# Kernel tuning notes

Hardware: AMD Instinct MI355X
Metric: run time of the kernel (lower is better)

## Reference

```python
import jax, jax.numpy as jnp
import numpy as np

F, HE, HD, A = 128, 512, 512, 256
B, T = 32, 512

def _uniform(key, shape, k):
    return jax.random.uniform(key, shape, jnp.float32, -k, k)

def setup_inputs() -> dict:
    key = jax.random.key(0)
    ks = jax.random.split(key, 20)
    ke = 1.0 / np.sqrt(HE)
    kd = 1.0 / np.sqrt(HD)
    ka = 1.0 / np.sqrt(A)
    kf = 1.0 / np.sqrt(F)
    return {
        "x": jax.random.normal(ks[0], (B, T, F), jnp.float32),
        # encoder LSTM (torch gate order i,f,g,o)
        "enc_Wih": _uniform(ks[1], (4 * HE, F), ke),
        "enc_Whh": _uniform(ks[2], (4 * HE, HE), ke),
        "enc_bih": _uniform(ks[3], (4 * HE,), ke),
        "enc_bhh": _uniform(ks[4], (4 * HE,), ke),
        # attention
        "Wenc_w": _uniform(ks[5], (A, HE), 1.0 / np.sqrt(HE)),
        "Wenc_b": _uniform(ks[6], (A,), 1.0 / np.sqrt(HE)),
        "Wdec_w": _uniform(ks[7], (A, HD), kd),
        "Wdec_b": _uniform(ks[8], (A,), kd),
        "V_w": _uniform(ks[9], (1, A), ka),
        "V_b": _uniform(ks[10], (1,), ka),
        "attn_bias": _uniform(ks[11], (A,), kd),
        # decoder LSTMCell: input size HD+HE
        "dec_Wih": _uniform(ks[12], (4 * HD, HD + HE), kd),
        "dec_Whh": _uniform(ks[13], (4 * HD, HD), kd),
        "dec_bih": _uniform(ks[14], (4 * HD,), kd),
        "dec_bhh": _uniform(ks[15], (4 * HD,), kd),
    }

def _lstm_step(xw, h, c, Whh, bias, H):
    # xw = x @ Wih.T precomputed; bias = bih + bhh
    z = xw + h @ Whh.T + bias
    i, f, g, o = jnp.split(z, 4, axis=-1)
    i, f, o = jax.nn.sigmoid(i), jax.nn.sigmoid(f), jax.nn.sigmoid(o)
    g = jnp.tanh(g)
    c_new = f * c + i * g
    h_new = o * jnp.tanh(c_new)
    return h_new, c_new

def reference(x, enc_Wih, enc_Whh, enc_bih, enc_bhh,
              Wenc_w, Wenc_b, Wdec_w, Wdec_b, V_w, V_b, attn_bias,
              dec_Wih, dec_Whh, dec_bih, dec_bhh):
    nb, nt, _ = x.shape
    # ---- encoder LSTM ----
    xw = jnp.einsum('btf,gf->btg', x, enc_Wih)  # [B,T,4HE]
    enc_bias = enc_bih + enc_bhh
    def enc_step(carry, xw_t):
        h, c = carry
        h, c = _lstm_step(xw_t, h, c, enc_Whh, enc_bias, HE)
        return (h, c), h
    h0 = jnp.zeros((nb, HE), x.dtype)
    c0 = jnp.zeros((nb, HE), x.dtype)
    _, enc_states = jax.lax.scan(enc_step, (h0, c0), jnp.swapaxes(xw, 0, 1))
    enc_states = jnp.swapaxes(enc_states, 0, 1)  # [B,T,HE]

    # ---- initial decoder step: zero input, zero state ----
    dec_bias = dec_bih + dec_bhh
    z0 = jnp.broadcast_to(dec_bias, (nb, 4 * HD))
    i, f, g, o = jnp.split(z0, 4, axis=-1)
    cdec = jax.nn.sigmoid(i) * jnp.tanh(g)
    hdec = jax.nn.sigmoid(o) * jnp.tanh(cdec)

    # precompute encoder projection for attention (math identical to per-step)
    enc_proj = jnp.einsum('bte,ae->bta', enc_states, Wenc_w) + Wenc_b  # [B,T,A]

    def dec_step(carry, _):
        h, c = carry
        dscore = h @ Wdec_w.T + Wdec_b  # [B,A]
        align = jnp.tanh(enc_proj + dscore[:, None, :] + attn_bias)  # [B,T,A]
        logits = jnp.einsum('bta,a->bt', align, V_w[0]) + V_b[0]
        w = jax.nn.softmax(logits, axis=-1)  # [B,T]
        ctx = jnp.einsum('bt,bte->be', w, enc_states)  # [B,HE]
        dec_in = jnp.concatenate([ctx, h], axis=-1)
        h, c = _lstm_step(dec_in @ dec_Wih.T, h, c, dec_Whh, dec_bias, HD)
        return (h, c), h
    _, outs = jax.lax.scan(dec_step, (hdec, cdec), None, length=nt)
    return jnp.swapaxes(outs, 0, 1)  # [B,T,HD]
```

## Files before the change

### kernel.cpp

```cpp
#include <hip/hip_runtime.h>
#include <stdint.h>

#define DEV __device__ __forceinline__

namespace {

constexpr int kT = 512, kB = 32, kF = 128, kHE = 512, kHD = 512, kA = 256;

typedef _Float16 f16;
typedef _Float16 h4 __attribute__((ext_vector_type(4)));
typedef unsigned long long u64;

constexpr size_t oWdecC  = 0;
constexpr size_t oWdWH   = oWdecC + 1048576;
constexpr size_t oEncSt  = oWdWH + 65536;
constexpr size_t oEncPr  = oEncSt + (size_t)kB*kT*kHE;
constexpr size_t oHdec   = oEncPr + (size_t)kB*kT*kA;
constexpr size_t oCtx    = oHdec + 3ull*kB*kHD;
constexpr size_t oDen    = oCtx + 3ull*kB*kHE;
constexpr size_t oScp    = oDen + 96;
constexpr size_t oEbias  = oScp + (size_t)kB*16*kA;
constexpr size_t oDbias  = oEbias + 2048;
constexpr size_t oAb2    = oDbias + 2048;
constexpr size_t oCtr    = oAb2 + 256;
constexpr size_t oHenc   = oCtr + 2048;
constexpr size_t oCtxP   = oEncSt;
constexpr size_t oDenP   = oEncSt + 3ull*32*16*512;

constexpr float kScale = 1.0f/64.0f;

DEV float frcp(float x){ return __builtin_amdgcn_rcpf(x); }
DEV float fsig(float x){ return frcp(1.f + __expf(-x)); }
DEV float ftanh(float x){ return 1.f - 2.f*frcp(__expf(2.f*x) + 1.f); }

DEV float ld_na(const float* p){ return __hip_atomic_load((float*)p, __ATOMIC_RELAXED, __HIP_MEMORY_SCOPE_AGENT); }
DEV void  st_na(float* p, float v){ __hip_atomic_store(p, v, __ATOMIC_RELAXED, __HIP_MEMORY_SCOPE_AGENT); }
DEV int   ld_ni(const int* p){ return __hip_atomic_load((int*)p, __ATOMIC_RELAXED, __HIP_MEMORY_SCOPE_AGENT); }
DEV void  st_ni(int* p, int v){ __hip_atomic_store(p, v, __ATOMIC_RELAXED, __HIP_MEMORY_SCOPE_AGENT); }
DEV float2 ld_na2(const float* p){
  u64 v = __hip_atomic_load((const u64*)p, __ATOMIC_RELAXED, __HIP_MEMORY_SCOPE_AGENT);
  union { u64 u; float2 f; } cv; cv.u = v; return cv.f;
}
DEV void st_na2(float* p, float2 v){
  union { float2 f; u64 u; } cv; cv.f = v;
  __hip_atomic_store((u64*)p, cv.u, __ATOMIC_RELAXED, __HIP_MEMORY_SCOPE_AGENT);
}

DEV void wait_slots(const int* base, int cnt, int tgt, int* abortf){
  if (threadIdx.x < 64){
    int lane = threadIdx.x;
    int guard = 0;
    for (;;){
      int ok = 1;
      for (int i = lane; i < cnt; i += 64) ok &= (ld_ni(base + i) >= tgt);
      if (__all(ok)) break;
      if (ld_ni(abortf) != 0) break;
      if (++guard > (1<<21)){ st_ni(abortf, 1); break; }
      __builtin_amdgcn_s_sleep(1);
    }
  }
  __syncthreads();
}
DEV void wait_count(const int* p, int tgt, int* abortf){
  if (threadIdx.x < 64){
    int guard = 0;
    for (;;){
      if (ld_ni(p) >= tgt) break;
      if (ld_ni(abortf) != 0) break;
      if (++guard > (1<<21)){ st_ni(abortf, 1); break; }
      __builtin_amdgcn_s_sleep(2);
    }
  }
  __syncthreads();
}
DEV void stamp_slot(int* slot, int v){
  __syncthreads();
  if (threadIdx.x == 0) st_ni(slot, v);
}

}

__global__ __launch_bounds__(256) void init_kernel(
    const float* __restrict__ eBih, const float* __restrict__ eBhh,
    const float* __restrict__ WdecW, const float* __restrict__ WdecB, const float* __restrict__ attnB,
    const float* __restrict__ dWih, const float* __restrict__ dWhh,
    const float* __restrict__ dBih, const float* __restrict__ dBhh,
    float* __restrict__ ws)
{
  float* whc = ws + oWdecC;
  f16* wdwh  = (f16*)(ws + oWdWH);
  float* hdec  = ws + oHdec;
  float* ebias = ws + oEbias;
  float* dbias = ws + oDbias;
  float* ab2w  = ws + oAb2;
  float* henc  = ws + oHenc;
  const int gid = blockIdx.x*256 + threadIdx.x;
  const int stride = gridDim.x*256;
  for (int i=gid; i<2048*512; i+=stride){
    int col = i>>9, k = i&511;
    whc[i] = dWih[((size_t)col<<10) + 512 + k] + dWhh[((size_t)col<<9) + k];
  }
  for (int i=gid; i<256*512; i+=stride)  wdwh[i] = (f16)WdecW[i];
  for (int i=gid; i<2048; i+=stride){ ebias[i] = eBih[i]+eBhh[i]; dbias[i] = dBih[i]+dBhh[i]; }
  for (int i=gid; i<256; i+=stride)  ab2w[i] = WdecB[i]+attnB[i];
  for (int i=gid; i<2*kB*kHE; i+=stride) henc[i] = 0.f;
  for (int i=gid; i<kB*kHD; i+=stride){
    int e = i & 511;
    float zi = dBih[e]+dBhh[e];
    float zg = dBih[1024+e]+dBhh[1024+e];
    float zo = dBih[1536+e]+dBhh[1536+e];
    float c0 = fsig(zi)*ftanh(zg);
    hdec[i] = fsig(zo)*ftanh(c0);
  }
}

__global__ __launch_bounds__(256, 1) void enc_kernel(
    const float* __restrict__ x, const float* __restrict__ eWih,
    const float* __restrict__ eWhh, float* __restrict__ ws)
{
  constexpr int WP = 644;
  constexpr int XP = 648;
  __shared__ float wsm[32*WP];
  __shared__ float xh[8*XP];
  __shared__ float zs[8][32];
  const float* ebias = ws + oEbias;
  float* encst = ws + oEncSt;
  float* henc  = ws + oHenc;
  int* ctr = (int*)(ws + oCtr);
  int* abortf = ctr;
  int* slotE = ctr + 1600;

  const int tid = threadIdx.x, bid = blockIdx.x;
  const int q = bid >> 6, j = bid & 63;
  const int b0 = q*8, e0 = j*8;

  for (int i = tid; i < 32*640; i += 256){
    int r = i / 640, k = i - r*640;
    int gate = r >> 3, el = r & 7;
    int grow = gate*kHE + e0 + el;
    float v = (k < kF) ? eWih[(size_t)grow*kF + k] : eWhh[(size_t)grow*kHE + (k - kF)];
    wsm[r*WP + k] = v;
  }
  const int b_l = tid >> 5, row = tid & 31;
  const float biasr = ebias[(row>>3)*kHE + e0 + (row&7)];
  const int b_p = tid >> 3, e_p = tid & 7;
  float creg = 0.f;
  __syncthreads();

  int p = 0;
  for (int t = 0; t < kT; ++t){
    {
      int bl2 = tid >> 5, q4 = tid & 31;
      *(float4*)(&xh[bl2*XP + 4*q4]) = ((const float4*)(x + ((size_t)(b0+bl2)*kT + t)*kF))[q4];
    }
    float a0=0.f, a1=0.f, a2=0.f, a3=0.f;
    {
      const float4* wr = (const float4*)(&wsm[row*WP]);
      const float4* xr = (const float4*)(&xh[b_l*XP]);
      #pragma unroll 8
      for (int kq = 0; kq < 32; ++kq){
        float4 w = wr[kq], v = xr[kq];
        a0 += w.x*v.x; a1 += w.y*v.y; a2 += w.z*v.z; a3 += w.w*v.w;
      }
    }
    wait_slots(slotE + q*64, 64, t, abortf);
    #pragma unroll
    for (int i = 0; i < 4; ++i){
      int idx = tid + 256*i;
      int bl2 = idx >> 7, q4 = idx & 127;
      const float* hsrc = henc + (size_t)p*kB*kHE + (size_t)(b0+bl2)*kHE + 4*q4;
      float2 h01 = ld_na2(hsrc), h23 = ld_na2(hsrc + 2);
      *(float4*)(&xh[bl2*XP + kF + 4*q4]) = make_float4(h01.x, h01.y, h23.x, h23.y);
    }
    __syncthreads();
    {
      const float4* wr = (const float4*)(&wsm[row*WP]);
      const float4* xr = (const float4*)(&xh[b_l*XP]);
      #pragma unroll 8
      for (int kq = 32; kq < 160; ++kq){
        float4 w = wr[kq], v = xr[kq];
        a0 += w.x*v.x; a1 += w.y*v.y; a2 += w.z*v.z; a3 += w.w*v.w;
      }
      zs[b_l][row] = (a0+a1)+(a2+a3) + biasr;
    }
    __syncthreads();
    if (tid < 64){
      float zi = zs[b_p][0*8 + e_p];
      float zf = zs[b_p][1*8 + e_p];
      float zg = zs[b_p][2*8 + e_p];
      float zo = zs[b_p][3*8 + e_p];
      float c2 = fsig(zf)*creg + fsig(zi)*ftanh(zg);
      creg = c2;
      float h = fsig(zo)*ftanh(c2);
      int b = b0 + b_p, e = e0 + e_p;
      st_na(&henc[(size_t)(p^1)*kB*kHE + (size_t)b*kHE + e], h);
      encst[((size_t)b*kT + t)*kHE + e] = h;
    }
    stamp_slot(&slotE[q*64 + j], t+1);
    p ^= 1;
  }
}

__global__ __launch_bounds__(256) void encproj_kernel(
    const float* __restrict__ WencW, const float* __restrict__ WencB,
    float* __restrict__ ws)
{
  const float* encst = ws + oEncSt;
  float* encpr = ws + oEncPr;
  __shared__ float4 et[32][32];
  const int tid = threadIdx.x, bid = blockIdx.x;
  const int r0 = bid*32;
  float acc[32];
  #pragma unroll
  for (int i=0;i<32;++i) acc[i]=0.f;
  for (int kt=0; kt<4; ++kt){
    #pragma unroll
    for (int i2=0;i2<4;++i2){
      int q = tid + i2*256;
      int row = q>>5, qi = q&31;
      et[row][qi] = ((const float4*)(encst + ((size_t)(r0+row))*kHE + kt*128))[qi];
    }
    __syncthreads();
    const float4* wv = (const float4*)(WencW + (size_t)tid*kHE + kt*128);
    #pragma unroll 1
    for (int q=0;q<32;++q){
      float4 w = wv[q];
      #pragma unroll
      for (int i=0;i<32;++i){
        float4 e4 = et[i][q];
        acc[i] += e4.x*w.x + e4.y*w.y + e4.z*w.z + e4.w*w.w;
      }
    }
    __syncthreads();
  }
  float bb = WencB[tid];
  #pragma unroll
  for (int i=0;i<32;++i) encpr[((size_t)(r0+i))*kA + tid] = acc[i] + bb;
}

namespace {
struct SA  { float h[32]; float sc[256]; float lw[32]; };
struct SC  { float xt[16][520]; float zb[128][2]; };
struct __align__(16) SmemDec {
  float wsl[8][1028];
  float v[256];
  SA a;
  SC c;
};
}

__global__ __launch_bounds__(256, 2) void dec_kernel(
    const float* __restrict__ Vw, const float* __restrict__ dWih,
    float* __restrict__ out, float* __restrict__ ws)
{
  __shared__ SmemDec sm;
  const int tid = threadIdx.x, bid = blockIdx.x;
  const float* whc = ws + oWdecC;
  const f16* wdwh  = (const f16*)(ws + oWdWH);
  const float* encst = ws + oEncSt;
  const float* encpr = ws + oEncPr;
  float* hdec = ws + oHdec;
  float* ctxb = ws + oCtx;
  float* den  = ws + oDen;
  float* scp  = ws + oScp;
  float* ctxp = ws + oCtxP;
  float* denp = ws + oDenP;
  const float* dbias = ws + oDbias;
  const float* ab2w  = ws + oAb2;
  int* ctr   = (int*)(ws + oCtr);
  int* abortf = ctr;
  int* startc = ctr + 16;
  int* slotC = ctr + 64;
  int* slotA = ctr + 576;
  int* slotB = ctr + 1088;
  int* slotR = ctr + 1856;

  const int bA = bid >> 4, tc = bid & 15, t0a = tc*32;
  const int half = bid >> 8, ecp = bid & 255, e0c = ecp*2;
  const bool isR = (tc == 0);
  const int col_l = tid & 127, ksC = tid >> 7;
  const int e_lC = col_l & 1, gateC = (col_l>>1)&3, b_lC = col_l>>3;
  const int wrow = gateC*2 + e_lC;

  for (int i = tid; i < 8*1024; i += 256){
    int rr = i >> 10, k = i & 1023;
    int col = (rr>>1)*kHD + e0c + (rr&1);
    float v = (k < 512) ? dWih[(size_t)col*1024 + k] : whc[(size_t)col*512 + (k-512)];
    sm.wsl[rr][k] = v;
  }
  sm.v[tid] = Vw[tid];

  h4 wA[8];
  { const h4* wv0 = (const h4*)(wdwh + (size_t)tid*kHD + t0a);
    #pragma unroll
    for (int q=0;q<8;++q) wA[q] = wv0[q]; }
  const int tl = tid>>3, as = tid&7;
  float4 eprR[8];
  { const float* eb2 = encpr + ((size_t)bA*kT + t0a + tl)*kA + as*4;
    #pragma unroll
    for (int q=0;q<8;++q) eprR[q] = *(const float4*)(eb2 + q*32); }
  float2 ev[32];
  { const float* eb = encst + ((size_t)bA*kT + t0a)*kHE + 2*tid;
    #pragma unroll
    for (int j=0;j<32;++j) ev[j] = *(const float2*)(eb + (size_t)j*kHE); }

  const float ab2r = ab2w[tid];
  float cregD=0, dbi=0, dbf=0, dbg=0, dbo=0;
  if (tid < 32){
    int e = e0c + (tid&1);
    dbi = dbias[e]; dbf = dbias[512+e]; dbg = dbias[1024+e]; dbo = dbias[1536+e];
    cregD = fsig(dbi)*ftanh(dbg);
  }
  __syncthreads();
  if (tid == 0) atomicAdd(startc, 1);
  wait_count(startc, 512, abortf);

  int r = 0;
  for (int t=0; t<kT; ++t){
    const int rn = (r==2) ? 0 : r+1;
    wait_slots(slotC + (bA>>4)*256 + tc*16, 16, t, abortf);
    if (tid < 32) sm.a.h[tid] = ld_na(hdec + (size_t)r*kB*kHD + (size_t)bA*kHD + t0a + tid);
    __syncthreads();
    {
      float sp = 0.f;
      #pragma unroll
      for (int q=0;q<8;++q){
        h4 w = wA[q];
        sp += (float)w.x*sm.a.h[q*4+0] + (float)w.y*sm.a.h[q*4+1]
            + (float)w.z*sm.a.h[q*4+2] + (float)w.w*sm.a.h[q*4+3];
      }
      st_na(&scp[((size_t)bA*16 + tc)*kA + tid], sp);
    }
    stamp_slot(&slotA[bA*16 + tc], t+1);
    wait_slots(slotA + bA*16, 16, t+1, abortf);
    {
      float sc = ab2r;
      #pragma unroll
      for (int j=0;j<16;++j) sc += ld_na(&scp[((size_t)bA*16 + j)*kA + tid]);
      sm.a.sc[tid] = sc;
    }
    __syncthreads();
    {
      float acc = 0.f;
      #pragma unroll
      for (int q=0;q<8;++q){
        int a0 = q*32 + as*4;
        float4 e4 = eprR[q];
        acc += sm.v[a0+0]*ftanh(e4.x + sm.a.sc[a0+0]);
        acc += sm.v[a0+1]*ftanh(e4.y + sm.a.sc[a0+1]);
        acc += sm.v[a0+2]*ftanh(e4.z + sm.a.sc[a0+2]);
        acc += sm.v[a0+3]*ftanh(e4.w + sm.a.sc[a0+3]);
      }
      acc += __shfl_down(acc, 4, 8);
      acc += __shfl_down(acc, 2, 8);
      acc += __shfl_down(acc, 1, 8);
      if (as == 0) sm.a.lw[tl] = __expf(acc) * kScale;
    }
    __syncthreads();
    {
      float c0=0.f, c1=0.f;
      #pragma unroll
      for (int j=0;j<32;++j){
        float w = sm.a.lw[j];
        c0 += w*ev[j].x; c1 += w*ev[j].y;
      }
      st_na2(&ctxp[(((size_t)r*kB + bA)*16 + tc)*kHE + 2*tid], make_float2(c0, c1));
      if (tid == 0){
        float ds = 0.f;
        #pragma unroll
        for (int j=0;j<32;++j) ds += sm.a.lw[j];
        st_na(&denp[((size_t)r*kB + bA)*16 + tc], ds);
      }
    }
    stamp_slot(&slotB[bA*16 + tc], t+1);
    if (isR){
      wait_slots(slotB + bA*16, 16, t+1, abortf);
      {
        const float* pb = ctxp + ((size_t)r*kB + bA)*16*kHE + 2*tid;
        float s0=0.f, s1=0.f;
        #pragma unroll
        for (int j=0;j<16;++j){
          float2 p = ld_na2(pb + (size_t)j*kHE);
          s0 += p.x; s1 += p.y;
        }
        st_na2(&ctxb[((size_t)r*kB + bA)*kHE + 2*tid], make_float2(s0, s1));
        float d = (tid < 16) ? ld_na(&denp[((size_t)r*kB + bA)*16 + tid]) : 0.f;
        d += __shfl_down(d, 8, 16);
        d += __shfl_down(d, 4, 16);
        d += __shfl_down(d, 2, 16);
        d += __shfl_down(d, 1, 16);
        if (tid == 0) st_na(&den[r*kB + bA], d);
      }
      stamp_slot(&slotR[bA], t+1);
    }
    wait_slots(slotC + half*256, 256, t, abortf);
    float acch = 0.f;
    {
      const float* hbase = hdec + (size_t)r*kB*kHD + (size_t)(half*16)*kHD + 2*tid;
      float2 hu[16];
      #pragma unroll
      for (int b=0;b<16;++b) hu[b] = ld_na2(hbase + (size_t)b*kHD);
      #pragma unroll
      for (int b=0;b<16;++b) *(float2*)(&sm.c.xt[b][2*tid]) = hu[b];
      __syncthreads();
      #pragma unroll
      for (int kc=2; kc<4; ++kc){
        const float4* wc4 = (const float4*)(&sm.wsl[wrow][kc*256 + ksC*128]);
        const float4* xv  = (const float4*)(&sm.c.xt[b_lC][(kc-2)*256 + ksC*128]);
        float a0=0.f, a1=0.f, a2=0.f, a3=0.f;
        #pragma unroll 8
        for (int q=0;q<32;++q){
          float4 w = wc4[q], v = xv[q];
          a0 += w.x*v.x; a1 += w.y*v.y; a2 += w.z*v.z; a3 += w.w*v.w;
        }
        acch += (a0+a1)+(a2+a3);
      }
      __syncthreads();
    }
    wait_slots(slotR + half*16, 16, t+1, abortf);
    {
      const float rv = frcp(ld_na(&den[r*kB + half*16 + b_lC]));
      const float* cbase = ctxb + (size_t)r*kB*kHE + (size_t)(half*16)*kHE + 2*tid;
      float2 cu[16];
      #pragma unroll
      for (int b=0;b<16;++b) cu[b] = ld_na2(cbase + (size_t)b*kHE);
      #pragma unroll
      for (int b=0;b<16;++b) *(float2*)(&sm.c.xt[b][2*tid]) = cu[b];
      __syncthreads();
      float accc = 0.f;
      #pragma unroll
      for (int kc=0; kc<2; ++kc){
        const float4* wc4 = (const float4*)(&sm.wsl[wrow][kc*256 + ksC*128]);
        const float4* xv  = (const float4*)(&sm.c.xt[b_lC][kc*256 + ksC*128]);
        float a0=0.f, a1=0.f, a2=0.f, a3=0.f;
        #pragma unroll 8
        for (int q=0;q<32;++q){
          float4 w = wc4[q], v = xv[q];
          a0 += w.x*v.x; a1 += w.y*v.y; a2 += w.z*v.z; a3 += w.w*v.w;
        }
        accc += (a0+a1)+(a2+a3);
      }
      sm.c.zb[col_l][ksC] = accc*rv + acch;
      __syncthreads();
      if (tid < 32){
        int base = (tid>>1)*8 + (tid&1);
        int e = e0c + (tid&1), b2 = half*16 + (tid>>1);
        float zi = sm.c.zb[base+0][0] + sm.c.zb[base+0][1] + dbi;
        float zf = sm.c.zb[base+2][0] + sm.c.zb[base+2][1] + dbf;
        float zg = sm.c.zb[base+4][0] + sm.c.zb[base+4][1] + dbg;
        float zo = sm.c.zb[base+6][0] + sm.c.zb[base+6][1] + dbo;
        float c2 = fsig(zf)*cregD + fsig(zi)*ftanh(zg);
        cregD = c2;
        float h = fsig(zo)*ftanh(c2);
        st_na(&hdec[(size_t)rn*kB*kHD + (size_t)b2*kHD + e], h);
        out[((size_t)b2*kT + t)*kHD + e] = h;
      }
    }
    stamp_slot(&slotC[half*256 + ecp], t+1);
    r = rn;
  }
}

extern "C" void kernel_launch(void* const* d_in, const int* in_sizes, int n_in,
                              void* d_out, int out_size, void* d_ws, size_t ws_size,
                              hipStream_t stream) {
  (void)in_sizes; (void)n_in; (void)out_size; (void)ws_size;
  const float* x     = (const float*)d_in[0];
  const float* eWih  = (const float*)d_in[1];
  const float* eWhh  = (const float*)d_in[2];
  const float* eBih  = (const float*)d_in[3];
  const float* eBhh  = (const float*)d_in[4];
  const float* WencW = (const float*)d_in[5];
  const float* WencB = (const float*)d_in[6];
  const float* WdecW = (const float*)d_in[7];
  const float* WdecB = (const float*)d_in[8];
  const float* Vw    = (const float*)d_in[9];
  const float* attnB = (const float*)d_in[11];
  const float* dWih  = (const float*)d_in[12];
  const float* dWhh  = (const float*)d_in[13];
  const float* dBih  = (const float*)d_in[14];
  const float* dBhh  = (const float*)d_in[15];
  float* ws = (float*)d_ws;
  int* ctr = (int*)(ws + oCtr);
  hipMemsetAsync(ctr, 0, 8192, stream);
  hipLaunchKernelGGL(init_kernel, dim3(512), dim3(256), 0, stream,
                     eBih, eBhh, WdecW, WdecB, attnB, dWih, dWhh, dBih, dBhh, ws);
  hipLaunchKernelGGL(enc_kernel, dim3(256), dim3(256), 0, stream, x, eWih, eWhh, ws);
  hipLaunchKernelGGL(encproj_kernel, dim3(512), dim3(256), 0, stream, WencW, WencB, ws);
  hipLaunchKernelGGL(dec_kernel, dim3(512), dim3(256), 0, stream, Vw, dWih, (float*)d_out, ws);
}
```

Baseline: 12.32 ms.

## Compute decoder score projection redundantly per block, dropping a cross-block barrier

```diff
diff --git a/kernel.cpp b/kernel.cpp
--- a/kernel.cpp
+++ b/kernel.cpp
@@ -88,7 +88,7 @@
     float* __restrict__ ws)
 {
   float* whc = ws + oWdecC;
-  f16* wdwh  = (f16*)(ws + oWdWH);
+  u64* wdT   = (u64*)(ws + oWdWH);
   float* hdec  = ws + oHdec;
   float* ebias = ws + oEbias;
   float* dbias = ws + oDbias;
@@ -100,7 +100,13 @@
     int col = i>>9, k = i&511;
     whc[i] = dWih[((size_t)col<<10) + 512 + k] + dWhh[((size_t)col<<9) + k];
   }
-  for (int i=gid; i<256*512; i+=stride)  wdwh[i] = (f16)WdecW[i];
+  for (int i=gid; i<64*256; i+=stride){
+    int c = i>>8, a = i&255;
+    const float* srcw = WdecW + (size_t)a*512 + 4*c;
+    union { u64 u; f16 h[4]; } pk4;
+    pk4.h[0]=(f16)srcw[0]; pk4.h[1]=(f16)srcw[1]; pk4.h[2]=(f16)srcw[2]; pk4.h[3]=(f16)srcw[3];
+    wdT[i] = pk4.u;
+  }
   for (int i=gid; i<2048; i+=stride){ ebias[i] = eBih[i]+eBhh[i]; dbias[i] = dBih[i]+dBhh[i]; }
   for (int i=gid; i<256; i+=stride)  ab2w[i] = WdecB[i]+attnB[i];
   for (int i=gid; i<2*kB*kHE; i+=stride) henc[i] = 0.f;
@@ -239,7 +245,7 @@
 }
 
 namespace {
-struct SA  { float h[32]; float sc[256]; float lw[32]; };
+struct SA  { float hs[512]; float sc[256]; float lw[32]; };
 struct SC  { float xt[16][520]; float zb[128][2]; };
 struct __align__(16) SmemDec {
   float wsl[8][1028];
@@ -256,13 +262,12 @@
   __shared__ SmemDec sm;
   const int tid = threadIdx.x, bid = blockIdx.x;
   const float* whc = ws + oWdecC;
-  const f16* wdwh  = (const f16*)(ws + oWdWH);
+  const u64* wdT   = (const u64*)(ws + oWdWH);
   const float* encst = ws + oEncSt;
   const float* encpr = ws + oEncPr;
   float* hdec = ws + oHdec;
   float* ctxb = ws + oCtx;
   float* den  = ws + oDen;
-  float* scp  = ws + oScp;
   float* ctxp = ws + oCtxP;
   float* denp = ws + oDenP;
   const float* dbias = ws + oDbias;
@@ -271,7 +276,6 @@
   int* abortf = ctr;
   int* startc = ctr + 16;
   int* slotC = ctr + 64;
-  int* slotA = ctr + 576;
   int* slotB = ctr + 1088;
   int* slotR = ctr + 1856;
 
@@ -290,10 +294,6 @@
   }
   sm.v[tid] = Vw[tid];
 
-  h4 wA[8];
-  { const h4* wv0 = (const h4*)(wdwh + (size_t)tid*kHD + t0a);
-    #pragma unroll
-    for (int q=0;q<8;++q) wA[q] = wv0[q]; }
   const int tl = tid>>3, as = tid&7;
   float4 eprR[8];
   { const float* eb2 = encpr + ((size_t)bA*kT + t0a + tl)*kA + as*4;
@@ -318,25 +318,26 @@
   int r = 0;
   for (int t=0; t<kT; ++t){
     const int rn = (r==2) ? 0 : r+1;
-    wait_slots(slotC + (bA>>4)*256 + tc*16, 16, t, abortf);
-    if (tid < 32) sm.a.h[tid] = ld_na(hdec + (size_t)r*kB*kHD + (size_t)bA*kHD + t0a + tid);
-    __syncthreads();
-    {
-      float sp = 0.f;
-      #pragma unroll
-      for (int q=0;q<8;++q){
-        h4 w = wA[q];
-        sp += (float)w.x*sm.a.h[q*4+0] + (float)w.y*sm.a.h[q*4+1]
-            + (float)w.z*sm.a.h[q*4+2] + (float)w.w*sm.a.h[q*4+3];
-      }
-      st_na(&scp[((size_t)bA*16 + tc)*kA + tid], sp);
-    }
-    stamp_slot(&slotA[bA*16 + tc], t+1);
-    wait_slots(slotA + bA*16, 16, t+1, abortf);
+    wait_slots(slotC + half*256, 256, t, abortf);
+    {
+      float2 hv = ld_na2(hdec + (size_t)r*kB*kHD + (size_t)bA*kHD + 2*tid);
+      *(float2*)(&sm.a.hs[2*tid]) = hv;
+    }
+    __syncthreads();
     {
       float sc = ab2r;
-      #pragma unroll
-      for (int j=0;j<16;++j) sc += ld_na(&scp[((size_t)bA*16 + j)*kA + tid]);
+      #pragma unroll 4
+      for (int j=0;j<16;++j){
+        float sp = 0.f;
+        #pragma unroll
+        for (int q=0;q<8;++q){
+          union { u64 u; h4 w; } cw; cw.u = wdT[(j*8+q)*256 + tid];
+          const int k0 = j*32 + q*4;
+          sp += (float)cw.w.x*sm.a.hs[k0+0] + (float)cw.w.y*sm.a.hs[k0+1]
+              + (float)cw.w.z*sm.a.hs[k0+2] + (float)cw.w.w*sm.a.hs[k0+3];
+        }
+        sc += sp;
+      }
       sm.a.sc[tid] = sc;
     }
     __syncthreads();
@@ -393,7 +394,6 @@
       }
       stamp_slot(&slotR[bA], t+1);
     }
-    wait_slots(slotC + half*256, 256, t, abortf);
     float acch = 0.f;
     {
       const float* hbase = hdec + (size_t)r*kB*kHD + (size_t)(half*16)*kHD + 2*tid;
```

Measured after the change: 17.34 ms. 40.7% more time.
